# Optimization experiments

Measured on AMD Instinct MI355X. Metric: run time of the kernel, lower is better.

Reference implementation:

```python
import jax, jax.numpy as jnp
import numpy as np

B, N, E, ED, H, HID, OUT = 128, 100, 3200, 8, 4, 16, 32


def _ln(x, g, b):
    m = x.mean(-1, keepdims=True)
    v = ((x - m) ** 2).mean(-1, keepdims=True)
    return (x - m) / jnp.sqrt(v + 1e-5) * g + b


def _seg_softmax(logits, seg, n):
    # logits: [Etot, H], seg: [Etot] target node ids
    m = jax.ops.segment_max(logits, seg, num_segments=n)
    ex = jnp.exp(logits - m[seg])
    s = jax.ops.segment_sum(ex, seg, num_segments=n)
    return ex / (s[seg] + 1e-16)


def _tconv(x, src, dst, ea, Wq, bq, Wk, bk, Wv, bv, We, Ws, bs, heads, ch, n):
    # PyG TransformerConv, concat=False, root_weight=True, beta=False
    q = (x @ Wq.T + bq).reshape(-1, heads, ch)
    k = (x @ Wk.T + bk).reshape(-1, heads, ch)
    v = (x @ Wv.T + bv).reshape(-1, heads, ch)
    e = (ea @ We.T).reshape(-1, heads, ch)
    alpha = (q[dst] * (k[src] + e)).sum(-1) / jnp.sqrt(jnp.float32(ch))  # [Etot,H]
    alpha = _seg_softmax(alpha, dst, n)
    msg = (v[src] + e) * alpha[..., None]
    out = jax.ops.segment_sum(msg, dst, num_segments=n)  # [n,H,ch]
    out = out.mean(axis=1)  # concat=False -> head mean
    return out + x @ Ws.T + bs


def setup_inputs() -> dict:
    key = jax.random.key(0)
    ks = jax.random.split(key, 32)
    d = {}
    d['nodes_feats'] = jax.random.randint(ks[0], (B, N, 1), 0, 5).astype(jnp.float32)
    d['edge_index'] = jax.random.randint(ks[1], (B, 2, E), 0, N).astype(jnp.int32)
    d['edge_attr'] = jax.random.normal(ks[2], (B, E, ED), jnp.float32)
    d['agent_id'] = jax.random.randint(ks[3], (B, 1), 0, N).astype(jnp.int32)
    s = 0.1
    d['entity_embed'] = jax.random.normal(ks[4], (5, 4), jnp.float32)
    d['W1'] = jax.random.normal(ks[5], (HID, 4 + ED), jnp.float32) * s
    d['b1'] = jnp.zeros((HID,), jnp.float32)
    d['W2'] = jax.random.normal(ks[6], (HID, HID), jnp.float32) * s
    d['b2'] = jnp.zeros((HID,), jnp.float32)
    d['W3'] = jax.random.normal(ks[7], (HID, HID), jnp.float32) * s
    d['b3'] = jnp.zeros((HID,), jnp.float32)
    d['ln_g'] = jnp.ones((HID,), jnp.float32)
    d['ln_b'] = jnp.zeros((HID,), jnp.float32)
    i = 8
    for pre, ch, outd in (('g1', HID, HID), ('g2', OUT, OUT)):
        d[pre + '_Wq'] = jax.random.normal(ks[i + 0], (H * ch, HID), jnp.float32) * s
        d[pre + '_bq'] = jnp.zeros((H * ch,), jnp.float32)
        d[pre + '_Wk'] = jax.random.normal(ks[i + 1], (H * ch, HID), jnp.float32) * s
        d[pre + '_bk'] = jnp.zeros((H * ch,), jnp.float32)
        d[pre + '_Wv'] = jax.random.normal(ks[i + 2], (H * ch, HID), jnp.float32) * s
        d[pre + '_bv'] = jnp.zeros((H * ch,), jnp.float32)
        d[pre + '_We'] = jax.random.normal(ks[i + 3], (H * ch, ED), jnp.float32) * s
        d[pre + '_Ws'] = jax.random.normal(ks[i + 4], (outd, HID), jnp.float32) * s
        d[pre + '_bs'] = jnp.zeros((outd,), jnp.float32)
        i += 5
    return d


def reference(nodes_feats, edge_index, edge_attr, agent_id, entity_embed,
              W1, b1, W2, b2, W3, b3, ln_g, ln_b,
              g1_Wq, g1_bq, g1_Wk, g1_bk, g1_Wv, g1_bv, g1_We, g1_Ws, g1_bs,
              g2_Wq, g2_bq, g2_Wk, g2_bk, g2_Wv, g2_bv, g2_We, g2_Ws, g2_bs):
    n_tot = B * N
    # batched graph -> flat graph with per-batch node offsets
    offs = (jnp.arange(B, dtype=edge_index.dtype) * N)[:, None, None]
    ei = (edge_index + offs).transpose(1, 0, 2).reshape(2, -1)  # [2, B*E]
    src, dst = ei[0], ei[1]
    x = nodes_feats.reshape(-1, 1)            # [n_tot, 1]
    ea = edge_attr.reshape(-1, ED)            # [B*E, ED]

    # Embedding message-passing layer (aggr='add')
    etype = x[:, 0].astype(jnp.int32)[src]
    emb = entity_embed[etype]                  # [Etot, 4]
    h = jnp.concatenate([emb, ea], axis=1)
    h = _ln(jax.nn.relu(h @ W1.T + b1), ln_g, ln_b)
    h = _ln(jax.nn.relu(h @ W2.T + b2), ln_g, ln_b)
    h = _ln(jax.nn.relu(h @ W3.T + b3), ln_g, ln_b)
    z = jax.ops.segment_sum(h, dst, num_segments=n_tot)  # [n_tot, 16]

    a = _tconv(z, src, dst, ea, g1_Wq, g1_bq, g1_Wk, g1_bk, g1_Wv, g1_bv,
               g1_We, g1_Ws, g1_bs, H, HID, n_tot)
    a = _tconv(a, src, dst, ea, g2_Wq, g2_bq, g2_Wk, g2_bk, g2_Wv, g2_bv,
               g2_We, g2_Ws, g2_bs, H, OUT, n_tot)
    a = jax.nn.relu(a).reshape(B, N, OUT)
    # graph_aggr == 'agent': gather the agent node per batch
    out = jnp.take_along_axis(a, agent_id[:, :, None].astype(jnp.int32), axis=1)
    return out[:, 0, :]  # [B, OUT]
```

## Files before the change

kernel.cpp:

```cpp
#include <hip/hip_runtime.h>
#include <math.h>
#include <stdint.h>

#define Bb   128
#define Nn   100
#define Ee   3200
#define NTOT (Bb*Nn)
#define ETOT (Bb*Ee)



__global__ __launch_bounds__(256) void k_csr(const int* __restrict__ ei,
                                             const int* __restrict__ agent,
                                             int* __restrict__ off,
                                             int2* __restrict__ cpair,
                                             int* __restrict__ mark)
{
    int b = ((blockIdx.x & 7) << 4) + (blockIdx.x >> 3);
    int t = threadIdx.x;
    __shared__ int cnt[128];
    __shared__ int exc[128];
    __shared__ int cur[128];
    if (t < 128) cnt[t] = 0;
    if (t < Nn) mark[b * Nn + t] = 0;
    __syncthreads();
    const int* eis = ei + (size_t)b * 2 * Ee;
    const int* eid = eis + Ee;
    for (int e = t; e < Ee; e += 256) atomicAdd(&cnt[eid[e]], 1);
    __syncthreads();
    if (t < 128) exc[t] = cnt[t];
    __syncthreads();
    for (int d = 1; d < 128; d <<= 1) {
        int v = 0;
        if (t < 128 && t >= d) v = exc[t - d];
        __syncthreads();
        if (t < 128) exc[t] += v;
        __syncthreads();
    }
    if (t < 128) { int e0 = exc[t] - cnt[t]; exc[t] = e0; cur[t] = e0; }
    __syncthreads();
    if (t < Nn) off[b * Nn + t] = b * Ee + exc[t];
    if (b == Bb - 1 && t == 0) off[NTOT] = ETOT;
    for (int e = t; e < Ee; e += 256) {
        int dst = eid[e];
        int idx = atomicAdd(&cur[dst], 1);
        cpair[b * Ee + idx] = make_int2(eis[e] + b * Nn, b * Ee + e);
    }
    int an = agent[b];
    __syncthreads();
    if (t == 0) mark[b * Nn + an] = 1;
    for (int e = t; e < Ee; e += 256) {
        if (eid[e] == an) mark[b * Nn + eis[e]] = 1;
    }
}


__device__ __forceinline__ void ln_reg(float* h, const float* __restrict__ g,
                                       const float* __restrict__ b) {
    float s = 0.f;
#pragma unroll
    for (int c = 0; c < 16; c++) s += h[c];
    float m = s * 0.0625f;
    float v = 0.f;
#pragma unroll
    for (int c = 0; c < 16; c++) { float d = h[c] - m; v += d * d; }
    float r = rsqrtf(v * 0.0625f + 1e-5f);
#pragma unroll
    for (int c = 0; c < 16; c++) h[c] = (h[c] - m) * r * g[c] + b[c];
}

__global__ __launch_bounds__(256) void k_mlpz(
    const float* __restrict__ nf, const float* __restrict__ ea, const float* __restrict__ ee,
    const float* __restrict__ W1, const float* __restrict__ b1,
    const float* __restrict__ W2, const float* __restrict__ b2,
    const float* __restrict__ W3, const float* __restrict__ b3,
    const float* __restrict__ lg, const float* __restrict__ lb,
    const float* __restrict__ Wq, const float* __restrict__ bq,
    const float* __restrict__ Wk, const float* __restrict__ bk,
    const float* __restrict__ Wv, const float* __restrict__ bv,
    const int* __restrict__ off, const int2* __restrict__ cpair,
    float* __restrict__ z, float* __restrict__ q1, float* __restrict__ k1, float* __restrict__ v1)
{
    __shared__ float hs[4][64][17];
    __shared__ int sdeg[4];
    int lane = threadIdx.x & 63;
    int wid  = threadIdx.x >> 6;
    int n    = (blockIdx.x & 7) * (NTOT / 8) + (blockIdx.x >> 3) * 4 + wid;

    int o0 = off[n];
    int deg = off[n + 1] - o0;
    if (lane == 0) sdeg[wid] = deg;
    __syncthreads();
    int mdeg = max(max(sdeg[0], sdeg[1]), max(sdeg[2], sdeg[3]));
    int chunks = (mdeg + 63) >> 6;

    float zp = 0.f;
    for (int ch = 0; ch < chunks; ch++) {
        int i = ch * 64 + lane;
        float h3[16];
        if (i < deg) {
            int2 p = cpair[o0 + i];
            int et = (int)nf[p.x];
            float in[12];
#pragma unroll
            for (int j = 0; j < 4; j++) in[j] = ee[et * 4 + j];
            const float4* ea4 = (const float4*)(ea + (size_t)p.y * 8);
            float4 ua = ea4[0], ub = ea4[1];
            in[4] = ua.x; in[5] = ua.y; in[6] = ua.z; in[7] = ua.w;
            in[8] = ub.x; in[9] = ub.y; in[10] = ub.z; in[11] = ub.w;

            float h1[16];
#pragma unroll
            for (int c = 0; c < 16; c++) {
                float s = b1[c];
#pragma unroll
                for (int j = 0; j < 12; j++) s = fmaf(W1[c * 12 + j], in[j], s);
                h1[c] = fmaxf(s, 0.f);
            }
            ln_reg(h1, lg, lb);
            float h2[16];
#pragma unroll
            for (int c = 0; c < 16; c++) {
                float s = b2[c];
#pragma unroll
                for (int j = 0; j < 16; j++) s = fmaf(W2[c * 16 + j], h1[j], s);
                h2[c] = fmaxf(s, 0.f);
            }
            ln_reg(h2, lg, lb);
#pragma unroll
            for (int c = 0; c < 16; c++) {
                float s = b3[c];
#pragma unroll
                for (int j = 0; j < 16; j++) s = fmaf(W3[c * 16 + j], h2[j], s);
                h3[c] = fmaxf(s, 0.f);
            }
            ln_reg(h3, lg, lb);
        } else {
#pragma unroll
            for (int c = 0; c < 16; c++) h3[c] = 0.f;
        }
#pragma unroll
        for (int c = 0; c < 16; c++) hs[wid][lane][c] = h3[c];
        __syncthreads();
        int g = lane >> 4, c = lane & 15;
        float s = 0.f;
#pragma unroll
        for (int k = 0; k < 16; k++) s += hs[wid][g * 16 + k][c];
        s += __shfl_xor(s, 16);
        s += __shfl_xor(s, 32);
        zp += s;
        __syncthreads();
    }

    if (lane < 16) z[n * 16 + lane] = zp;

    float aq = bq[lane], ak = bk[lane], av = bv[lane];
#pragma unroll
    for (int j = 0; j < 16; j++) {
        float zj = __shfl(zp, j, 16);
        aq = fmaf(Wq[lane * 16 + j], zj, aq);
        ak = fmaf(Wk[lane * 16 + j], zj, ak);
        av = fmaf(Wv[lane * 16 + j], zj, av);
    }
    q1[n * 64 + lane] = aq;
    k1[n * 64 + lane] = ak;
    v1[n * 64 + lane] = av;
}


__global__ __launch_bounds__(256) void k_attn1(
    const float* __restrict__ ea,
    const float* __restrict__ q1, const float* __restrict__ k1, const float* __restrict__ v1,
    const float* __restrict__ We, const float* __restrict__ Ws, const float* __restrict__ bs,
    const float* __restrict__ z, const int* __restrict__ mark,
    const int* __restrict__ off, const int2* __restrict__ cpair,
    float* __restrict__ a1)
{
    int lane = threadIdx.x & 63;
    int wid  = threadIdx.x >> 6;
    int n    = (blockIdx.x & 7) * (NTOT / 8) + (blockIdx.x >> 3) * 4 + wid;

    if (!mark[n]) return;

    float wer[8];
#pragma unroll
    for (int j = 0; j < 8; j++) wer[j] = We[lane * 8 + j];
    float ql = q1[n * 64 + lane];

    int o0 = off[n];
    int deg = off[n + 1] - o0;

    float m = -1e30f, l = 0.f, acc = 0.f;
    int i = 0;
    for (; i + 2 <= deg; i += 2) {
        int2 pA = cpair[o0 + i];
        int2 pB = cpair[o0 + i + 1];
        const float4* eaA = (const float4*)(ea + (size_t)pA.y * 8);
        const float4* eaB = (const float4*)(ea + (size_t)pB.y * 8);
        float4 a0v = eaA[0], a1v = eaA[1], b0v = eaB[0], b1v = eaB[1];
        float eA = wer[0] * a0v.x + wer[1] * a0v.y + wer[2] * a0v.z + wer[3] * a0v.w
                 + wer[4] * a1v.x + wer[5] * a1v.y + wer[6] * a1v.z + wer[7] * a1v.w;
        float eB = wer[0] * b0v.x + wer[1] * b0v.y + wer[2] * b0v.z + wer[3] * b0v.w
                 + wer[4] * b1v.x + wer[5] * b1v.y + wer[6] * b1v.z + wer[7] * b1v.w;
        float kA = k1[(size_t)pA.x * 64 + lane];
        float kB = k1[(size_t)pB.x * 64 + lane];
        float vA = v1[(size_t)pA.x * 64 + lane];
        float vB = v1[(size_t)pB.x * 64 + lane];
        float tA = ql * (kA + eA);
        float tB = ql * (kB + eB);
        tA += __shfl_xor(tA, 1, 16);  tB += __shfl_xor(tB, 1, 16);
        tA += __shfl_xor(tA, 2, 16);  tB += __shfl_xor(tB, 2, 16);
        tA += __shfl_xor(tA, 4, 16);  tB += __shfl_xor(tB, 4, 16);
        tA += __shfl_xor(tA, 8, 16);  tB += __shfl_xor(tB, 8, 16);
        float lA = tA * 0.25f;
        float lB = tB * 0.25f;
        float nm = fmaxf(m, fmaxf(lA, lB));
        float sc = __expf(m - nm);
        float wA = __expf(lA - nm);
        float wB = __expf(lB - nm);
        acc = acc * sc + wA * (vA + eA) + wB * (vB + eB);
        l   = l * sc + wA + wB;
        m   = nm;
    }
    for (; i < deg; i++) {
        int2 p = cpair[o0 + i];
        const float4* ea4 = (const float4*)(ea + (size_t)p.y * 8);
        float4 u0 = ea4[0], u1 = ea4[1];
        float el = wer[0] * u0.x + wer[1] * u0.y + wer[2] * u0.z + wer[3] * u0.w
                 + wer[4] * u1.x + wer[5] * u1.y + wer[6] * u1.z + wer[7] * u1.w;
        float kl = k1[(size_t)p.x * 64 + lane];
        float t = ql * (kl + el);
        t += __shfl_xor(t, 1, 16);
        t += __shfl_xor(t, 2, 16);
        t += __shfl_xor(t, 4, 16);
        t += __shfl_xor(t, 8, 16);
        float logit = t * 0.25f;
        float nm = fmaxf(m, logit);
        float sc = __expf(m - nm);
        float w  = __expf(logit - nm);
        float vl = v1[(size_t)p.x * 64 + lane];
        acc = acc * sc + w * (vl + el);
        l   = l * sc + w;
        m   = nm;
    }
    float y = (deg > 0) ? (acc / l) : 0.f;
    y += __shfl_xor(y, 16);
    y += __shfl_xor(y, 32);
    y *= 0.25f;

    if (lane < 16) {
        float r = bs[lane];
#pragma unroll
        for (int j = 0; j < 16; j++) r = fmaf(Ws[lane * 16 + j], z[n * 16 + j], r);
        a1[n * 16 + lane] = y + r;
    }
}


__global__ __launch_bounds__(256) void k_g2(
    const float* __restrict__ ea, const float* __restrict__ a1, const int* __restrict__ agent,
    const float* __restrict__ Wq, const float* __restrict__ bq,
    const float* __restrict__ Wk, const float* __restrict__ bk,
    const float* __restrict__ Wv, const float* __restrict__ bv,
    const float* __restrict__ We, const float* __restrict__ Ws, const float* __restrict__ bs,
    const int* __restrict__ off, const int2* __restrict__ cpair,
    float* __restrict__ out)
{
    __shared__ float sm[4][64], sl[4][64], sa0[4][64], sa1[4][64];
    int b = ((blockIdx.x & 7) << 4) + (blockIdx.x >> 3);
    int lane = threadIdx.x & 63;
    int w = threadIdx.x >> 6;
    int n = b * Nn + agent[b];
    int v0 = lane * 2, v1i = lane * 2 + 1;

    float aa[16];
#pragma unroll
    for (int j = 0; j < 16; j++) aa[j] = a1[n * 16 + j];

    float wk0[16], wk1[16], wv0[16], wv1[16], we0[8], we1[8];
#pragma unroll
    for (int j = 0; j < 16; j++) {
        wk0[j] = Wk[v0 * 16 + j];  wk1[j] = Wk[v1i * 16 + j];
        wv0[j] = Wv[v0 * 16 + j];  wv1[j] = Wv[v1i * 16 + j];
    }
#pragma unroll
    for (int j = 0; j < 8; j++) { we0[j] = We[v0 * 8 + j]; we1[j] = We[v1i * 8 + j]; }

    float q0 = bq[v0], q1v = bq[v1i];
#pragma unroll
    for (int j = 0; j < 16; j++) {
        q0  = fmaf(Wq[v0 * 16 + j],  aa[j], q0);
        q1v = fmaf(Wq[v1i * 16 + j], aa[j], q1v);
    }

    int o0 = off[n];
    int deg = off[n + 1] - o0;

    float m = -1e30f, l = 0.f, a0 = 0.f, a1c = 0.f;
    for (int i = w; i < deg; i += 4) {
        int2 p = cpair[o0 + i];
        int src = p.x, ge = p.y;
        float as[16];
#pragma unroll
        for (int j = 0; j < 16; j++) as[j] = a1[src * 16 + j];
        const float4* ea4 = (const float4*)(ea + (size_t)ge * 8);
        float4 u0 = ea4[0], u1 = ea4[1];
        float eav[8] = {u0.x, u0.y, u0.z, u0.w, u1.x, u1.y, u1.z, u1.w};

        float k0 = bk[v0], k1v = bk[v1i], vv0 = bv[v0], vv1 = bv[v1i];
#pragma unroll
        for (int j = 0; j < 16; j++) {
            k0  = fmaf(wk0[j], as[j], k0);
            k1v = fmaf(wk1[j], as[j], k1v);
            vv0 = fmaf(wv0[j], as[j], vv0);
            vv1 = fmaf(wv1[j], as[j], vv1);
        }
        float e0 = 0.f, e1 = 0.f;
#pragma unroll
        for (int j = 0; j < 8; j++) { e0 = fmaf(we0[j], eav[j], e0); e1 = fmaf(we1[j], eav[j], e1); }

        float t = q0 * (k0 + e0) + q1v * (k1v + e1);
        t += __shfl_xor(t, 1, 16);
        t += __shfl_xor(t, 2, 16);
        t += __shfl_xor(t, 4, 16);
        t += __shfl_xor(t, 8, 16);
        float logit = t * 0.17677669529663687f;
        float nm = fmaxf(m, logit);
        float sc = __expf(m - nm);
        float wgt = __expf(logit - nm);
        a0  = a0 * sc + wgt * (vv0 + e0);
        a1c = a1c * sc + wgt * (vv1 + e1);
        l   = l * sc + wgt;
        m   = nm;
    }
    sm[w][lane] = m; sl[w][lane] = l; sa0[w][lane] = a0; sa1[w][lane] = a1c;
    __syncthreads();
    if (w == 0) {
        float M = fmaxf(fmaxf(sm[0][lane], sm[1][lane]), fmaxf(sm[2][lane], sm[3][lane]));
        float L = 0.f, A0 = 0.f, A1 = 0.f;
#pragma unroll
        for (int ww = 0; ww < 4; ww++) {
            float sc = __expf(sm[ww][lane] - M);
            L  += sc * sl[ww][lane];
            A0 += sc * sa0[ww][lane];
            A1 += sc * sa1[ww][lane];
        }
        float y0 = (deg > 0) ? (A0 / L) : 0.f;
        float y1 = (deg > 0) ? (A1 / L) : 0.f;
        y0 += __shfl_xor(y0, 16); y0 += __shfl_xor(y0, 32);
        y1 += __shfl_xor(y1, 16); y1 += __shfl_xor(y1, 32);
        y0 *= 0.25f; y1 *= 0.25f;

        if (lane < 16) {
            int c0 = lane * 2, c1 = lane * 2 + 1;
            float r0 = bs[c0], r1 = bs[c1];
#pragma unroll
            for (int j = 0; j < 16; j++) {
                r0 = fmaf(Ws[c0 * 16 + j], aa[j], r0);
                r1 = fmaf(Ws[c1 * 16 + j], aa[j], r1);
            }
            out[b * 32 + c0] = fmaxf(y0 + r0, 0.f);
            out[b * 32 + c1] = fmaxf(y1 + r1, 0.f);
        }
    }
}


extern "C" void kernel_launch(void* const* d_in, const int* in_sizes, int n_in,
                              void* d_out, int out_size, void* d_ws, size_t ws_size,
                              hipStream_t stream) {
    (void)in_sizes; (void)n_in; (void)out_size; (void)ws_size;
    const float* nf    = (const float*)d_in[0];
    const int*   ei    = (const int*)d_in[1];
    const float* ea    = (const float*)d_in[2];
    const int*   agent = (const int*)d_in[3];
    const float* ee    = (const float*)d_in[4];
    const float* W1    = (const float*)d_in[5];
    const float* b1    = (const float*)d_in[6];
    const float* W2    = (const float*)d_in[7];
    const float* b2    = (const float*)d_in[8];
    const float* W3    = (const float*)d_in[9];
    const float* b3    = (const float*)d_in[10];
    const float* lg    = (const float*)d_in[11];
    const float* lb    = (const float*)d_in[12];
    const float* g1Wq  = (const float*)d_in[13];
    const float* g1bq  = (const float*)d_in[14];
    const float* g1Wk  = (const float*)d_in[15];
    const float* g1bk  = (const float*)d_in[16];
    const float* g1Wv  = (const float*)d_in[17];
    const float* g1bv  = (const float*)d_in[18];
    const float* g1We  = (const float*)d_in[19];
    const float* g1Ws  = (const float*)d_in[20];
    const float* g1bs  = (const float*)d_in[21];
    const float* g2Wq  = (const float*)d_in[22];
    const float* g2bq  = (const float*)d_in[23];
    const float* g2Wk  = (const float*)d_in[24];
    const float* g2bk  = (const float*)d_in[25];
    const float* g2Wv  = (const float*)d_in[26];
    const float* g2bv  = (const float*)d_in[27];
    const float* g2We  = (const float*)d_in[28];
    const float* g2Ws  = (const float*)d_in[29];
    const float* g2bs  = (const float*)d_in[30];
    float* out = (float*)d_out;

    char* w = (char*)d_ws;
    int* mark  = (int*)w;  w += (size_t)NTOT * 4;
    int* off   = (int*)w;  w += (size_t)(NTOT + 4) * 4;
    w = (char*)(((uintptr_t)w + 15) & ~(uintptr_t)15);
    int2* cpair = (int2*)w; w += (size_t)ETOT * 8;
    float* z   = (float*)w; w += (size_t)NTOT * 16 * 4;
    float* q1  = (float*)w; w += (size_t)NTOT * 64 * 4;
    float* k1  = (float*)w; w += (size_t)NTOT * 64 * 4;
    float* v1  = (float*)w; w += (size_t)NTOT * 64 * 4;
    float* a1  = (float*)w; w += (size_t)NTOT * 16 * 4;

    k_csr<<<dim3(Bb), dim3(256), 0, stream>>>(ei, agent, off, cpair, mark);
    k_mlpz<<<dim3(NTOT / 4), dim3(256), 0, stream>>>(
        nf, ea, ee, W1, b1, W2, b2, W3, b3, lg, lb,
        g1Wq, g1bq, g1Wk, g1bk, g1Wv, g1bv,
        off, cpair, z, q1, k1, v1);
    k_attn1<<<dim3(NTOT / 4), dim3(256), 0, stream>>>(
        ea, q1, k1, v1, g1We, g1Ws, g1bs, z, mark, off, cpair, a1);
    k_g2<<<dim3(Bb), dim3(256), 0, stream>>>(
        ea, a1, agent, g2Wq, g2bq, g2Wk, g2bk, g2Wv, g2bv, g2We, g2Ws, g2bs,
        off, cpair, out);
}
```

Measured before the change: 206.7 us.

## Fuse layer-1 attention and layer-2 agent conv into one per-graph kernel

Merges the per-node first attention kernel and the per-graph second conv kernel into a single per-graph block of 512 threads. Each block stages the graph's k, v, z and CSR pairs in shared memory, and computes q on the fly, which removes the q1 and a1 global buffers and one launch. The CSR build also stages the edge indices in shared memory so global memory is read once. The cost is that only 128 blocks run the attention work, and each wave walks several marked nodes serially, which lowers parallelism.

```diff
diff --git a/kernel.cpp b/kernel.cpp
--- a/kernel.cpp
+++ b/kernel.cpp
@@ -10,7 +10,7 @@
 
 
 
-__global__ __launch_bounds__(256) void k_csr(const int* __restrict__ ei,
+__global__ __launch_bounds__(512) void k_csr(const int* __restrict__ ei,
                                              const int* __restrict__ agent,
                                              int* __restrict__ off,
                                              int2* __restrict__ cpair,
@@ -18,6 +18,8 @@
 {
     int b = ((blockIdx.x & 7) << 4) + (blockIdx.x >> 3);
     int t = threadIdx.x;
+    __shared__ int s_src[Ee];
+    __shared__ int s_dst[Ee];
     __shared__ int cnt[128];
     __shared__ int exc[128];
     __shared__ int cur[128];
@@ -26,7 +28,13 @@
     __syncthreads();
     const int* eis = ei + (size_t)b * 2 * Ee;
     const int* eid = eis + Ee;
-    for (int e = t; e < Ee; e += 256) atomicAdd(&cnt[eid[e]], 1);
+    for (int e = t; e < Ee; e += 512) {
+        int s = eis[e];
+        int d = eid[e];
+        s_src[e] = s;
+        s_dst[e] = d;
+        atomicAdd(&cnt[d], 1);
+    }
     __syncthreads();
     if (t < 128) exc[t] = cnt[t];
     __syncthreads();
@@ -41,16 +49,15 @@
     __syncthreads();
     if (t < Nn) off[b * Nn + t] = b * Ee + exc[t];
     if (b == Bb - 1 && t == 0) off[NTOT] = ETOT;
-    for (int e = t; e < Ee; e += 256) {
-        int dst = eid[e];
-        int idx = atomicAdd(&cur[dst], 1);
-        cpair[b * Ee + idx] = make_int2(eis[e] + b * Nn, b * Ee + e);
+    for (int e = t; e < Ee; e += 512) {
+        int d = s_dst[e];
+        int idx = atomicAdd(&cur[d], 1);
+        cpair[b * Ee + idx] = make_int2(s_src[e] + b * Nn, b * Ee + e);
     }
     int an = agent[b];
-    __syncthreads();
     if (t == 0) mark[b * Nn + an] = 1;
-    for (int e = t; e < Ee; e += 256) {
-        if (eid[e] == an) mark[b * Nn + eis[e]] = 1;
+    for (int e = t; e < Ee; e += 512) {
+        if (s_dst[e] == an) mark[b * Nn + s_src[e]] = 1;
     }
 }
 
@@ -75,11 +82,10 @@
     const float* __restrict__ W2, const float* __restrict__ b2,
     const float* __restrict__ W3, const float* __restrict__ b3,
     const float* __restrict__ lg, const float* __restrict__ lb,
-    const float* __restrict__ Wq, const float* __restrict__ bq,
     const float* __restrict__ Wk, const float* __restrict__ bk,
     const float* __restrict__ Wv, const float* __restrict__ bv,
     const int* __restrict__ off, const int2* __restrict__ cpair,
-    float* __restrict__ z, float* __restrict__ q1, float* __restrict__ k1, float* __restrict__ v1)
+    float* __restrict__ z, float* __restrict__ k1, float* __restrict__ v1)
 {
     __shared__ float hs[4][64][17];
     __shared__ int sdeg[4];
@@ -154,160 +160,187 @@
 
     if (lane < 16) z[n * 16 + lane] = zp;
 
-    float aq = bq[lane], ak = bk[lane], av = bv[lane];
+    float ak = bk[lane], av = bv[lane];
 #pragma unroll
     for (int j = 0; j < 16; j++) {
         float zj = __shfl(zp, j, 16);
-        aq = fmaf(Wq[lane * 16 + j], zj, aq);
         ak = fmaf(Wk[lane * 16 + j], zj, ak);
         av = fmaf(Wv[lane * 16 + j], zj, av);
     }
-    q1[n * 64 + lane] = aq;
     k1[n * 64 + lane] = ak;
     v1[n * 64 + lane] = av;
 }
 
 
-__global__ __launch_bounds__(256) void k_attn1(
+__global__ __launch_bounds__(512) void k_attn(
     const float* __restrict__ ea,
-    const float* __restrict__ q1, const float* __restrict__ k1, const float* __restrict__ v1,
-    const float* __restrict__ We, const float* __restrict__ Ws, const float* __restrict__ bs,
+    const float* __restrict__ k1, const float* __restrict__ v1,
     const float* __restrict__ z, const int* __restrict__ mark,
+    const int* __restrict__ agent,
     const int* __restrict__ off, const int2* __restrict__ cpair,
-    float* __restrict__ a1)
+    const float* __restrict__ g1Wq, const float* __restrict__ g1bq,
+    const float* __restrict__ g1We, const float* __restrict__ g1Ws, const float* __restrict__ g1bs,
+    const float* __restrict__ g2Wq, const float* __restrict__ g2bq,
+    const float* __restrict__ g2Wk, const float* __restrict__ g2bk,
+    const float* __restrict__ g2Wv, const float* __restrict__ g2bv,
+    const float* __restrict__ g2We, const float* __restrict__ g2Ws, const float* __restrict__ g2bs,
+    float* __restrict__ out)
 {
-    int lane = threadIdx.x & 63;
-    int wid  = threadIdx.x >> 6;
-    int n    = (blockIdx.x & 7) * (NTOT / 8) + (blockIdx.x >> 3) * 4 + wid;
-
-    if (!mark[n]) return;
-
-    float wer[8];
-#pragma unroll
-    for (int j = 0; j < 8; j++) wer[j] = We[lane * 8 + j];
-    float ql = q1[n * 64 + lane];
-
-    int o0 = off[n];
-    int deg = off[n + 1] - o0;
-
-    float m = -1e30f, l = 0.f, acc = 0.f;
-    int i = 0;
-    for (; i + 2 <= deg; i += 2) {
-        int2 pA = cpair[o0 + i];
-        int2 pB = cpair[o0 + i + 1];
-        const float4* eaA = (const float4*)(ea + (size_t)pA.y * 8);
-        const float4* eaB = (const float4*)(ea + (size_t)pB.y * 8);
-        float4 a0v = eaA[0], a1v = eaA[1], b0v = eaB[0], b1v = eaB[1];
-        float eA = wer[0] * a0v.x + wer[1] * a0v.y + wer[2] * a0v.z + wer[3] * a0v.w
-                 + wer[4] * a1v.x + wer[5] * a1v.y + wer[6] * a1v.z + wer[7] * a1v.w;
-        float eB = wer[0] * b0v.x + wer[1] * b0v.y + wer[2] * b0v.z + wer[3] * b0v.w
-                 + wer[4] * b1v.x + wer[5] * b1v.y + wer[6] * b1v.z + wer[7] * b1v.w;
-        float kA = k1[(size_t)pA.x * 64 + lane];
-        float kB = k1[(size_t)pB.x * 64 + lane];
-        float vA = v1[(size_t)pA.x * 64 + lane];
-        float vB = v1[(size_t)pB.x * 64 + lane];
-        float tA = ql * (kA + eA);
-        float tB = ql * (kB + eB);
-        tA += __shfl_xor(tA, 1, 16);  tB += __shfl_xor(tB, 1, 16);
-        tA += __shfl_xor(tA, 2, 16);  tB += __shfl_xor(tB, 2, 16);
-        tA += __shfl_xor(tA, 4, 16);  tB += __shfl_xor(tB, 4, 16);
-        tA += __shfl_xor(tA, 8, 16);  tB += __shfl_xor(tB, 8, 16);
-        float lA = tA * 0.25f;
-        float lB = tB * 0.25f;
-        float nm = fmaxf(m, fmaxf(lA, lB));
-        float sc = __expf(m - nm);
-        float wA = __expf(lA - nm);
-        float wB = __expf(lB - nm);
-        acc = acc * sc + wA * (vA + eA) + wB * (vB + eB);
-        l   = l * sc + wA + wB;
-        m   = nm;
-    }
-    for (; i < deg; i++) {
-        int2 p = cpair[o0 + i];
+    __shared__ alignas(16) float sk[Nn][64];
+    __shared__ alignas(16) float sv[Nn][64];
+    __shared__ alignas(16) int2  spair[Ee];
+    __shared__ alignas(16) float sz[Nn][16];
+    __shared__ float a1s[Nn][16];
+    __shared__ int   soff[Nn + 1];
+    __shared__ int   smark[Nn];
+    __shared__ float sm2[8][64], sl2[8][64], sa0[8][64], sa1[8][64];
+
+    int b = ((blockIdx.x & 7) << 4) + (blockIdx.x >> 3);
+    int t = threadIdx.x;
+    int lane = t & 63;
+    int wid  = t >> 6;
+
+    const float4* kg = (const float4*)(k1 + (size_t)b * Nn * 64);
+    const float4* vg = (const float4*)(v1 + (size_t)b * Nn * 64);
+    const float4* zg = (const float4*)(z  + (size_t)b * Nn * 16);
+    float4* skd = (float4*)&sk[0][0];
+    float4* svd = (float4*)&sv[0][0];
+    float4* szd = (float4*)&sz[0][0];
+    for (int i = t; i < Nn * 16; i += 512) { skd[i] = kg[i]; svd[i] = vg[i]; }
+    for (int i = t; i < Nn * 4; i += 512) szd[i] = zg[i];
+    const int2* cg = cpair + (size_t)b * Ee;
+    for (int i = t; i < Ee; i += 512) spair[i] = cg[i];
+    if (t <= Nn) soff[t] = off[b * Nn + t] - b * Ee;
+    if (t < Nn) smark[t] = mark[b * Nn + t];
+    __syncthreads();
+
+    float wq[16], wer[8], ws1[16];
+#pragma unroll
+    for (int j = 0; j < 16; j++) wq[j] = g1Wq[lane * 16 + j];
+#pragma unroll
+    for (int j = 0; j < 8; j++) wer[j] = g1We[lane * 8 + j];
+    float bq1 = g1bq[lane];
+    int lc = lane & 15;
+#pragma unroll
+    for (int j = 0; j < 16; j++) ws1[j] = g1Ws[lc * 16 + j];
+    float bs1 = g1bs[lc];
+
+    for (int loc = wid; loc < Nn; loc += 8) {
+        if (!smark[loc]) continue;
+        float zz[16];
+#pragma unroll
+        for (int j = 0; j < 16; j++) zz[j] = sz[loc][j];
+        float ql = bq1;
+#pragma unroll
+        for (int j = 0; j < 16; j++) ql = fmaf(wq[j], zz[j], ql);
+
+        int o0 = soff[loc];
+        int deg = soff[loc + 1] - o0;
+
+        float m = -1e30f, l = 0.f, acc = 0.f;
+        int i = 0;
+        for (; i + 2 <= deg; i += 2) {
+            int2 pA = spair[o0 + i];
+            int2 pB = spair[o0 + i + 1];
+            const float4* eaA = (const float4*)(ea + (size_t)pA.y * 8);
+            const float4* eaB = (const float4*)(ea + (size_t)pB.y * 8);
+            float4 a0v = eaA[0], a1v = eaA[1], b0v = eaB[0], b1v = eaB[1];
+            float eA = wer[0] * a0v.x + wer[1] * a0v.y + wer[2] * a0v.z + wer[3] * a0v.w
+                     + wer[4] * a1v.x + wer[5] * a1v.y + wer[6] * a1v.z + wer[7] * a1v.w;
+            float eB = wer[0] * b0v.x + wer[1] * b0v.y + wer[2] * b0v.z + wer[3] * b0v.w
+                     + wer[4] * b1v.x + wer[5] * b1v.y + wer[6] * b1v.z + wer[7] * b1v.w;
+            int la = pA.x - b * Nn, lB = pB.x - b * Nn;
+            float kA = sk[la][lane], kB = sk[lB][lane];
+            float vA = sv[la][lane], vB = sv[lB][lane];
+            float tA = ql * (kA + eA);
+            float tB = ql * (kB + eB);
+            tA += __shfl_xor(tA, 1, 16);  tB += __shfl_xor(tB, 1, 16);
+            tA += __shfl_xor(tA, 2, 16);  tB += __shfl_xor(tB, 2, 16);
+            tA += __shfl_xor(tA, 4, 16);  tB += __shfl_xor(tB, 4, 16);
+            tA += __shfl_xor(tA, 8, 16);  tB += __shfl_xor(tB, 8, 16);
+            float lA = tA * 0.25f;
+            float lBv = tB * 0.25f;
+            float nm = fmaxf(m, fmaxf(lA, lBv));
+            float sc = __expf(m - nm);
+            float wA = __expf(lA - nm);
+            float wB = __expf(lBv - nm);
+            acc = acc * sc + wA * (vA + eA) + wB * (vB + eB);
+            l   = l * sc + wA + wB;
+            m   = nm;
+        }
+        for (; i < deg; i++) {
+            int2 p = spair[o0 + i];
+            const float4* ea4 = (const float4*)(ea + (size_t)p.y * 8);
+            float4 u0 = ea4[0], u1 = ea4[1];
+            float el = wer[0] * u0.x + wer[1] * u0.y + wer[2] * u0.z + wer[3] * u0.w
+                     + wer[4] * u1.x + wer[5] * u1.y + wer[6] * u1.z + wer[7] * u1.w;
+            int ls = p.x - b * Nn;
+            float kl = sk[ls][lane];
+            float tq = ql * (kl + el);
+            tq += __shfl_xor(tq, 1, 16);
+            tq += __shfl_xor(tq, 2, 16);
+            tq += __shfl_xor(tq, 4, 16);
+            tq += __shfl_xor(tq, 8, 16);
+            float logit = tq * 0.25f;
+            float nm = fmaxf(m, logit);
+            float sc = __expf(m - nm);
+            float w  = __expf(logit - nm);
+            float vl = sv[ls][lane];
+            acc = acc * sc + w * (vl + el);
+            l   = l * sc + w;
+            m   = nm;
+        }
+        float y = (deg > 0) ? (acc / l) : 0.f;
+        y += __shfl_xor(y, 16);
+        y += __shfl_xor(y, 32);
+        y *= 0.25f;
+        if (lane < 16) {
+            float r = bs1;
+#pragma unroll
+            for (int j = 0; j < 16; j++) r = fmaf(ws1[j], zz[j], r);
+            a1s[loc][lane] = y + r;
+        }
+    }
+    __syncthreads();
+
+    int an = agent[b];
+    int v0 = lane * 2, v1i = lane * 2 + 1;
+
+    float aa[16];
+#pragma unroll
+    for (int j = 0; j < 16; j++) aa[j] = a1s[an][j];
+
+    float wk0[16], wk1[16], wv0[16], wv1[16], we0[8], we1[8];
+#pragma unroll
+    for (int j = 0; j < 16; j++) {
+        wk0[j] = g2Wk[v0 * 16 + j];  wk1[j] = g2Wk[v1i * 16 + j];
+        wv0[j] = g2Wv[v0 * 16 + j];  wv1[j] = g2Wv[v1i * 16 + j];
+    }
+#pragma unroll
+    for (int j = 0; j < 8; j++) { we0[j] = g2We[v0 * 8 + j]; we1[j] = g2We[v1i * 8 + j]; }
+
+    float q0 = g2bq[v0], q1v = g2bq[v1i];
+#pragma unroll
+    for (int j = 0; j < 16; j++) {
+        q0  = fmaf(g2Wq[v0 * 16 + j],  aa[j], q0);
+        q1v = fmaf(g2Wq[v1i * 16 + j], aa[j], q1v);
+    }
+
+    int o0a = soff[an];
+    int dega = soff[an + 1] - o0a;
+
+    float m = -1e30f, l = 0.f, a0 = 0.f, a1c = 0.f;
+    for (int i = wid; i < dega; i += 8) {
+        int2 p = spair[o0a + i];
+        int srcl = p.x - b * Nn;
+        float as[16];
+#pragma unroll
+        for (int j = 0; j < 16; j++) as[j] = a1s[srcl][j];
         const float4* ea4 = (const float4*)(ea + (size_t)p.y * 8);
         float4 u0 = ea4[0], u1 = ea4[1];
-        float el = wer[0] * u0.x + wer[1] * u0.y + wer[2] * u0.z + wer[3] * u0.w
-                 + wer[4] * u1.x + wer[5] * u1.y + wer[6] * u1.z + wer[7] * u1.w;
-        float kl = k1[(size_t)p.x * 64 + lane];
-        float t = ql * (kl + el);
-        t += __shfl_xor(t, 1, 16);
-        t += __shfl_xor(t, 2, 16);
-        t += __shfl_xor(t, 4, 16);
-        t += __shfl_xor(t, 8, 16);
-        float logit = t * 0.25f;
-        float nm = fmaxf(m, logit);
-        float sc = __expf(m - nm);
-        float w  = __expf(logit - nm);
-        float vl = v1[(size_t)p.x * 64 + lane];
-        acc = acc * sc + w * (vl + el);
-        l   = l * sc + w;
-        m   = nm;
-    }
-    float y = (deg > 0) ? (acc / l) : 0.f;
-    y += __shfl_xor(y, 16);
-    y += __shfl_xor(y, 32);
-    y *= 0.25f;
-
-    if (lane < 16) {
-        float r = bs[lane];
-#pragma unroll
-        for (int j = 0; j < 16; j++) r = fmaf(Ws[lane * 16 + j], z[n * 16 + j], r);
-        a1[n * 16 + lane] = y + r;
-    }
-}
-
-
-__global__ __launch_bounds__(256) void k_g2(
-    const float* __restrict__ ea, const float* __restrict__ a1, const int* __restrict__ agent,
-    const float* __restrict__ Wq, const float* __restrict__ bq,
-    const float* __restrict__ Wk, const float* __restrict__ bk,
-    const float* __restrict__ Wv, const float* __restrict__ bv,
-    const float* __restrict__ We, const float* __restrict__ Ws, const float* __restrict__ bs,
-    const int* __restrict__ off, const int2* __restrict__ cpair,
-    float* __restrict__ out)
-{
-    __shared__ float sm[4][64], sl[4][64], sa0[4][64], sa1[4][64];
-    int b = ((blockIdx.x & 7) << 4) + (blockIdx.x >> 3);
-    int lane = threadIdx.x & 63;
-    int w = threadIdx.x >> 6;
-    int n = b * Nn + agent[b];
-    int v0 = lane * 2, v1i = lane * 2 + 1;
-
-    float aa[16];
-#pragma unroll
-    for (int j = 0; j < 16; j++) aa[j] = a1[n * 16 + j];
-
-    float wk0[16], wk1[16], wv0[16], wv1[16], we0[8], we1[8];
-#pragma unroll
-    for (int j = 0; j < 16; j++) {
-        wk0[j] = Wk[v0 * 16 + j];  wk1[j] = Wk[v1i * 16 + j];
-        wv0[j] = Wv[v0 * 16 + j];  wv1[j] = Wv[v1i * 16 + j];
-    }
-#pragma unroll
-    for (int j = 0; j < 8; j++) { we0[j] = We[v0 * 8 + j]; we1[j] = We[v1i * 8 + j]; }
-
-    float q0 = bq[v0], q1v = bq[v1i];
-#pragma unroll
-    for (int j = 0; j < 16; j++) {
-        q0  = fmaf(Wq[v0 * 16 + j],  aa[j], q0);
-        q1v = fmaf(Wq[v1i * 16 + j], aa[j], q1v);
-    }
-
-    int o0 = off[n];
-    int deg = off[n + 1] - o0;
-
-    float m = -1e30f, l = 0.f, a0 = 0.f, a1c = 0.f;
-    for (int i = w; i < deg; i += 4) {
-        int2 p = cpair[o0 + i];
-        int src = p.x, ge = p.y;
-        float as[16];
-#pragma unroll
-        for (int j = 0; j < 16; j++) as[j] = a1[src * 16 + j];
-        const float4* ea4 = (const float4*)(ea + (size_t)ge * 8);
-        float4 u0 = ea4[0], u1 = ea4[1];
         float eav[8] = {u0.x, u0.y, u0.z, u0.w, u1.x, u1.y, u1.z, u1.w};
 
-        float k0 = bk[v0], k1v = bk[v1i], vv0 = bv[v0], vv1 = bv[v1i];
+        float k0 = g2bk[v0], k1v = g2bk[v1i], vv0 = g2bv[v0], vv1 = g2bv[v1i];
 #pragma unroll
         for (int j = 0; j < 16; j++) {
             k0  = fmaf(wk0[j], as[j], k0);
@@ -319,12 +352,12 @@
 #pragma unroll
         for (int j = 0; j < 8; j++) { e0 = fmaf(we0[j], eav[j], e0); e1 = fmaf(we1[j], eav[j], e1); }
 
-        float t = q0 * (k0 + e0) + q1v * (k1v + e1);
-        t += __shfl_xor(t, 1, 16);
-        t += __shfl_xor(t, 2, 16);
-        t += __shfl_xor(t, 4, 16);
-        t += __shfl_xor(t, 8, 16);
-        float logit = t * 0.17677669529663687f;
+        float tq = q0 * (k0 + e0) + q1v * (k1v + e1);
+        tq += __shfl_xor(tq, 1, 16);
+        tq += __shfl_xor(tq, 2, 16);
+        tq += __shfl_xor(tq, 4, 16);
+        tq += __shfl_xor(tq, 8, 16);
+        float logit = tq * 0.17677669529663687f;
         float nm = fmaxf(m, logit);
         float sc = __expf(m - nm);
         float wgt = __expf(logit - nm);
@@ -333,31 +366,33 @@
         l   = l * sc + wgt;
         m   = nm;
     }
-    sm[w][lane] = m; sl[w][lane] = l; sa0[w][lane] = a0; sa1[w][lane] = a1c;
-    __syncthreads();
-    if (w == 0) {
-        float M = fmaxf(fmaxf(sm[0][lane], sm[1][lane]), fmaxf(sm[2][lane], sm[3][lane]));
+    sm2[wid][lane] = m; sl2[wid][lane] = l; sa0[wid][lane] = a0; sa1[wid][lane] = a1c;
+    __syncthreads();
+    if (wid == 0) {
+        float M = sm2[0][lane];
+#pragma unroll
+        for (int ww = 1; ww < 8; ww++) M = fmaxf(M, sm2[ww][lane]);
         float L = 0.f, A0 = 0.f, A1 = 0.f;
 #pragma unroll
-        for (int ww = 0; ww < 4; ww++) {
-            float sc = __expf(sm[ww][lane] - M);
-            L  += sc * sl[ww][lane];
+        for (int ww = 0; ww < 8; ww++) {
+            float sc = __expf(sm2[ww][lane] - M);
+            L  += sc * sl2[ww][lane];
             A0 += sc * sa0[ww][lane];
             A1 += sc * sa1[ww][lane];
         }
-        float y0 = (deg > 0) ? (A0 / L) : 0.f;
-        float y1 = (deg > 0) ? (A1 / L) : 0.f;
+        float y0 = (dega > 0) ? (A0 / L) : 0.f;
+        float y1 = (dega > 0) ? (A1 / L) : 0.f;
         y0 += __shfl_xor(y0, 16); y0 += __shfl_xor(y0, 32);
         y1 += __shfl_xor(y1, 16); y1 += __shfl_xor(y1, 32);
         y0 *= 0.25f; y1 *= 0.25f;
 
         if (lane < 16) {
             int c0 = lane * 2, c1 = lane * 2 + 1;
-            float r0 = bs[c0], r1 = bs[c1];
+            float r0 = g2bs[c0], r1 = g2bs[c1];
 #pragma unroll
             for (int j = 0; j < 16; j++) {
-                r0 = fmaf(Ws[c0 * 16 + j], aa[j], r0);
-                r1 = fmaf(Ws[c1 * 16 + j], aa[j], r1);
+                r0 = fmaf(g2Ws[c0 * 16 + j], aa[j], r0);
+                r1 = fmaf(g2Ws[c1 * 16 + j], aa[j], r1);
             }
             out[b * 32 + c0] = fmaxf(y0 + r0, 0.f);
             out[b * 32 + c1] = fmaxf(y1 + r1, 0.f);
@@ -409,19 +444,17 @@
     w = (char*)(((uintptr_t)w + 15) & ~(uintptr_t)15);
     int2* cpair = (int2*)w; w += (size_t)ETOT * 8;
     float* z   = (float*)w; w += (size_t)NTOT * 16 * 4;
-    float* q1  = (float*)w; w += (size_t)NTOT * 64 * 4;
     float* k1  = (float*)w; w += (size_t)NTOT * 64 * 4;
     float* v1  = (float*)w; w += (size_t)NTOT * 64 * 4;
-    float* a1  = (float*)w; w += (size_t)NTOT * 16 * 4;
-
-    k_csr<<<dim3(Bb), dim3(256), 0, stream>>>(ei, agent, off, cpair, mark);
+
+    k_csr<<<dim3(Bb), dim3(512), 0, stream>>>(ei, agent, off, cpair, mark);
     k_mlpz<<<dim3(NTOT / 4), dim3(256), 0, stream>>>(
         nf, ea, ee, W1, b1, W2, b2, W3, b3, lg, lb,
-        g1Wq, g1bq, g1Wk, g1bk, g1Wv, g1bv,
-        off, cpair, z, q1, k1, v1);
-    k_attn1<<<dim3(NTOT / 4), dim3(256), 0, stream>>>(
-        ea, q1, k1, v1, g1We, g1Ws, g1bs, z, mark, off, cpair, a1);
-    k_g2<<<dim3(Bb), dim3(256), 0, stream>>>(
-        ea, a1, agent, g2Wq, g2bq, g2Wk, g2bk, g2Wv, g2bv, g2We, g2Ws, g2bs,
-        off, cpair, out);
+        g1Wk, g1bk, g1Wv, g1bv,
+        off, cpair, z, k1, v1);
+    k_attn<<<dim3(Bb), dim3(512), 0, stream>>>(
+        ea, k1, v1, z, mark, agent, off, cpair,
+        g1Wq, g1bq, g1We, g1Ws, g1bs,
+        g2Wq, g2bq, g2Wk, g2bk, g2Wv, g2bv, g2We, g2Ws, g2bs,
+        out);
 }
```

New measurement: 236.3 us. +14.3%, slower.

## Split attention over waves per node, move Q projection into attention, stage CSR in LDS

Applied to the files above, without the earlier changes.

The CSR build kernel now uses 512 threads and stages src/dst indices in shared memory, so global edge indices are read only once. The first-layer attention kernel launches one block per node and splits that node's edges across four waves, then merges the partial online-softmax results through shared memory. Q is now computed only for marked nodes inside attention instead of for every node in the MLP kernel, which removes the q1 buffer writes. The second-layer kernel goes from 4 to 8 waves per graph. Exited unmarked blocks make the launch larger, and the extra shared-memory merge adds sync overhead.

```diff
diff --git a/kernel.cpp b/kernel.cpp
--- a/kernel.cpp
+++ b/kernel.cpp
@@ -10,7 +10,7 @@
 
 
 
-__global__ __launch_bounds__(256) void k_csr(const int* __restrict__ ei,
+__global__ __launch_bounds__(512) void k_csr(const int* __restrict__ ei,
                                              const int* __restrict__ agent,
                                              int* __restrict__ off,
                                              int2* __restrict__ cpair,
@@ -18,6 +18,8 @@
 {
     int b = ((blockIdx.x & 7) << 4) + (blockIdx.x >> 3);
     int t = threadIdx.x;
+    __shared__ int s_src[Ee];
+    __shared__ int s_dst[Ee];
     __shared__ int cnt[128];
     __shared__ int exc[128];
     __shared__ int cur[128];
@@ -26,7 +28,13 @@
     __syncthreads();
     const int* eis = ei + (size_t)b * 2 * Ee;
     const int* eid = eis + Ee;
-    for (int e = t; e < Ee; e += 256) atomicAdd(&cnt[eid[e]], 1);
+    for (int e = t; e < Ee; e += 512) {
+        int s = eis[e];
+        int d = eid[e];
+        s_src[e] = s;
+        s_dst[e] = d;
+        atomicAdd(&cnt[d], 1);
+    }
     __syncthreads();
     if (t < 128) exc[t] = cnt[t];
     __syncthreads();
@@ -41,16 +49,15 @@
     __syncthreads();
     if (t < Nn) off[b * Nn + t] = b * Ee + exc[t];
     if (b == Bb - 1 && t == 0) off[NTOT] = ETOT;
-    for (int e = t; e < Ee; e += 256) {
-        int dst = eid[e];
-        int idx = atomicAdd(&cur[dst], 1);
-        cpair[b * Ee + idx] = make_int2(eis[e] + b * Nn, b * Ee + e);
+    for (int e = t; e < Ee; e += 512) {
+        int d = s_dst[e];
+        int idx = atomicAdd(&cur[d], 1);
+        cpair[b * Ee + idx] = make_int2(s_src[e] + b * Nn, b * Ee + e);
     }
     int an = agent[b];
-    __syncthreads();
     if (t == 0) mark[b * Nn + an] = 1;
-    for (int e = t; e < Ee; e += 256) {
-        if (eid[e] == an) mark[b * Nn + eis[e]] = 1;
+    for (int e = t; e < Ee; e += 512) {
+        if (s_dst[e] == an) mark[b * Nn + s_src[e]] = 1;
     }
 }
 
@@ -75,11 +82,10 @@
     const float* __restrict__ W2, const float* __restrict__ b2,
     const float* __restrict__ W3, const float* __restrict__ b3,
     const float* __restrict__ lg, const float* __restrict__ lb,
-    const float* __restrict__ Wq, const float* __restrict__ bq,
     const float* __restrict__ Wk, const float* __restrict__ bk,
     const float* __restrict__ Wv, const float* __restrict__ bv,
     const int* __restrict__ off, const int2* __restrict__ cpair,
-    float* __restrict__ z, float* __restrict__ q1, float* __restrict__ k1, float* __restrict__ v1)
+    float* __restrict__ z, float* __restrict__ k1, float* __restrict__ v1)
 {
     __shared__ float hs[4][64][17];
     __shared__ int sdeg[4];
@@ -154,15 +160,13 @@
 
     if (lane < 16) z[n * 16 + lane] = zp;
 
-    float aq = bq[lane], ak = bk[lane], av = bv[lane];
+    float ak = bk[lane], av = bv[lane];
 #pragma unroll
     for (int j = 0; j < 16; j++) {
         float zj = __shfl(zp, j, 16);
-        aq = fmaf(Wq[lane * 16 + j], zj, aq);
         ak = fmaf(Wk[lane * 16 + j], zj, ak);
         av = fmaf(Wv[lane * 16 + j], zj, av);
     }
-    q1[n * 64 + lane] = aq;
     k1[n * 64 + lane] = ak;
     v1[n * 64 + lane] = av;
 }
@@ -170,31 +174,39 @@
 
 __global__ __launch_bounds__(256) void k_attn1(
     const float* __restrict__ ea,
-    const float* __restrict__ q1, const float* __restrict__ k1, const float* __restrict__ v1,
+    const float* __restrict__ k1, const float* __restrict__ v1,
+    const float* __restrict__ z, const int* __restrict__ mark,
+    const float* __restrict__ Wq, const float* __restrict__ bq,
     const float* __restrict__ We, const float* __restrict__ Ws, const float* __restrict__ bs,
-    const float* __restrict__ z, const int* __restrict__ mark,
     const int* __restrict__ off, const int2* __restrict__ cpair,
     float* __restrict__ a1)
 {
+    int n = (blockIdx.x & 7) * (NTOT / 8) + (blockIdx.x >> 3);
+    if (!mark[n]) return;
+
+    __shared__ float sm[4][64], sl[4][64], sa[4][64];
     int lane = threadIdx.x & 63;
-    int wid  = threadIdx.x >> 6;
-    int n    = (blockIdx.x & 7) * (NTOT / 8) + (blockIdx.x >> 3) * 4 + wid;
-
-    if (!mark[n]) return;
-
+    int w    = threadIdx.x >> 6;
+
+    float zz[16];
+#pragma unroll
+    for (int j = 0; j < 16; j++) zz[j] = z[n * 16 + j];
+    float ql = bq[lane];
+#pragma unroll
+    for (int j = 0; j < 16; j++) ql = fmaf(Wq[lane * 16 + j], zz[j], ql);
     float wer[8];
 #pragma unroll
     for (int j = 0; j < 8; j++) wer[j] = We[lane * 8 + j];
-    float ql = q1[n * 64 + lane];
-
-    int o0 = off[n];
+
+    int o0  = off[n];
     int deg = off[n + 1] - o0;
+    int i    = o0 + ((deg * w) >> 2);
+    int iend = o0 + ((deg * (w + 1)) >> 2);
 
     float m = -1e30f, l = 0.f, acc = 0.f;
-    int i = 0;
-    for (; i + 2 <= deg; i += 2) {
-        int2 pA = cpair[o0 + i];
-        int2 pB = cpair[o0 + i + 1];
+    for (; i + 2 <= iend; i += 2) {
+        int2 pA = cpair[i];
+        int2 pB = cpair[i + 1];
         const float4* eaA = (const float4*)(ea + (size_t)pA.y * 8);
         const float4* eaB = (const float4*)(ea + (size_t)pB.y * 8);
         float4 a0v = eaA[0], a1v = eaA[1], b0v = eaB[0], b1v = eaB[1];
@@ -212,52 +224,63 @@
         tA += __shfl_xor(tA, 2, 16);  tB += __shfl_xor(tB, 2, 16);
         tA += __shfl_xor(tA, 4, 16);  tB += __shfl_xor(tB, 4, 16);
         tA += __shfl_xor(tA, 8, 16);  tB += __shfl_xor(tB, 8, 16);
-        float lA = tA * 0.25f;
-        float lB = tB * 0.25f;
-        float nm = fmaxf(m, fmaxf(lA, lB));
+        float lA  = tA * 0.25f;
+        float lBv = tB * 0.25f;
+        float nm = fmaxf(m, fmaxf(lA, lBv));
         float sc = __expf(m - nm);
         float wA = __expf(lA - nm);
-        float wB = __expf(lB - nm);
+        float wB = __expf(lBv - nm);
         acc = acc * sc + wA * (vA + eA) + wB * (vB + eB);
         l   = l * sc + wA + wB;
         m   = nm;
     }
-    for (; i < deg; i++) {
-        int2 p = cpair[o0 + i];
+    for (; i < iend; i++) {
+        int2 p = cpair[i];
         const float4* ea4 = (const float4*)(ea + (size_t)p.y * 8);
         float4 u0 = ea4[0], u1 = ea4[1];
         float el = wer[0] * u0.x + wer[1] * u0.y + wer[2] * u0.z + wer[3] * u0.w
                  + wer[4] * u1.x + wer[5] * u1.y + wer[6] * u1.z + wer[7] * u1.w;
         float kl = k1[(size_t)p.x * 64 + lane];
-        float t = ql * (kl + el);
-        t += __shfl_xor(t, 1, 16);
-        t += __shfl_xor(t, 2, 16);
-        t += __shfl_xor(t, 4, 16);
-        t += __shfl_xor(t, 8, 16);
-        float logit = t * 0.25f;
+        float tq = ql * (kl + el);
+        tq += __shfl_xor(tq, 1, 16);
+        tq += __shfl_xor(tq, 2, 16);
+        tq += __shfl_xor(tq, 4, 16);
+        tq += __shfl_xor(tq, 8, 16);
+        float logit = tq * 0.25f;
         float nm = fmaxf(m, logit);
         float sc = __expf(m - nm);
-        float w  = __expf(logit - nm);
+        float wv = __expf(logit - nm);
         float vl = v1[(size_t)p.x * 64 + lane];
-        acc = acc * sc + w * (vl + el);
-        l   = l * sc + w;
+        acc = acc * sc + wv * (vl + el);
+        l   = l * sc + wv;
         m   = nm;
     }
-    float y = (deg > 0) ? (acc / l) : 0.f;
-    y += __shfl_xor(y, 16);
-    y += __shfl_xor(y, 32);
-    y *= 0.25f;
-
-    if (lane < 16) {
-        float r = bs[lane];
-#pragma unroll
-        for (int j = 0; j < 16; j++) r = fmaf(Ws[lane * 16 + j], z[n * 16 + j], r);
-        a1[n * 16 + lane] = y + r;
-    }
-}
-
-
-__global__ __launch_bounds__(256) void k_g2(
+    sm[w][lane] = m; sl[w][lane] = l; sa[w][lane] = acc;
+    __syncthreads();
+    if (w == 0) {
+        float M = fmaxf(fmaxf(sm[0][lane], sm[1][lane]), fmaxf(sm[2][lane], sm[3][lane]));
+        float L = 0.f, A = 0.f;
+#pragma unroll
+        for (int ww = 0; ww < 4; ww++) {
+            float sc = __expf(sm[ww][lane] - M);
+            L += sc * sl[ww][lane];
+            A += sc * sa[ww][lane];
+        }
+        float y = (deg > 0) ? (A / L) : 0.f;
+        y += __shfl_xor(y, 16);
+        y += __shfl_xor(y, 32);
+        y *= 0.25f;
+        if (lane < 16) {
+            float r = bs[lane];
+#pragma unroll
+            for (int j = 0; j < 16; j++) r = fmaf(Ws[lane * 16 + j], zz[j], r);
+            a1[n * 16 + lane] = y + r;
+        }
+    }
+}
+
+
+__global__ __launch_bounds__(512) void k_g2(
     const float* __restrict__ ea, const float* __restrict__ a1, const int* __restrict__ agent,
     const float* __restrict__ Wq, const float* __restrict__ bq,
     const float* __restrict__ Wk, const float* __restrict__ bk,
@@ -266,7 +289,7 @@
     const int* __restrict__ off, const int2* __restrict__ cpair,
     float* __restrict__ out)
 {
-    __shared__ float sm[4][64], sl[4][64], sa0[4][64], sa1[4][64];
+    __shared__ float sm[8][64], sl[8][64], sa0[8][64], sa1[8][64];
     int b = ((blockIdx.x & 7) << 4) + (blockIdx.x >> 3);
     int lane = threadIdx.x & 63;
     int w = threadIdx.x >> 6;
@@ -297,7 +320,7 @@
     int deg = off[n + 1] - o0;
 
     float m = -1e30f, l = 0.f, a0 = 0.f, a1c = 0.f;
-    for (int i = w; i < deg; i += 4) {
+    for (int i = w; i < deg; i += 8) {
         int2 p = cpair[o0 + i];
         int src = p.x, ge = p.y;
         float as[16];
@@ -336,10 +359,12 @@
     sm[w][lane] = m; sl[w][lane] = l; sa0[w][lane] = a0; sa1[w][lane] = a1c;
     __syncthreads();
     if (w == 0) {
-        float M = fmaxf(fmaxf(sm[0][lane], sm[1][lane]), fmaxf(sm[2][lane], sm[3][lane]));
+        float M = sm[0][lane];
+#pragma unroll
+        for (int ww = 1; ww < 8; ww++) M = fmaxf(M, sm[ww][lane]);
         float L = 0.f, A0 = 0.f, A1 = 0.f;
 #pragma unroll
-        for (int ww = 0; ww < 4; ww++) {
+        for (int ww = 0; ww < 8; ww++) {
             float sc = __expf(sm[ww][lane] - M);
             L  += sc * sl[ww][lane];
             A0 += sc * sa0[ww][lane];
@@ -409,19 +434,20 @@
     w = (char*)(((uintptr_t)w + 15) & ~(uintptr_t)15);
     int2* cpair = (int2*)w; w += (size_t)ETOT * 8;
     float* z   = (float*)w; w += (size_t)NTOT * 16 * 4;
-    float* q1  = (float*)w; w += (size_t)NTOT * 64 * 4;
     float* k1  = (float*)w; w += (size_t)NTOT * 64 * 4;
     float* v1  = (float*)w; w += (size_t)NTOT * 64 * 4;
     float* a1  = (float*)w; w += (size_t)NTOT * 16 * 4;
 
-    k_csr<<<dim3(Bb), dim3(256), 0, stream>>>(ei, agent, off, cpair, mark);
+    k_csr<<<dim3(Bb), dim3(512), 0, stream>>>(ei, agent, off, cpair, mark);
     k_mlpz<<<dim3(NTOT / 4), dim3(256), 0, stream>>>(
         nf, ea, ee, W1, b1, W2, b2, W3, b3, lg, lb,
-        g1Wq, g1bq, g1Wk, g1bk, g1Wv, g1bv,
-        off, cpair, z, q1, k1, v1);
-    k_attn1<<<dim3(NTOT / 4), dim3(256), 0, stream>>>(
-        ea, q1, k1, v1, g1We, g1Ws, g1bs, z, mark, off, cpair, a1);
-    k_g2<<<dim3(Bb), dim3(256), 0, stream>>>(
+        g1Wk, g1bk, g1Wv, g1bv,
+        off, cpair, z, k1, v1);
+    k_attn1<<<dim3(NTOT), dim3(256), 0, stream>>>(
+        ea, k1, v1, z, mark,
+        g1Wq, g1bq, g1We, g1Ws, g1bs,
+        off, cpair, a1);
+    k_g2<<<dim3(Bb), dim3(512), 0, stream>>>(
         ea, a1, agent, g2Wq, g2bq, g2Wk, g2bk, g2Wv, g2bv, g2We, g2Ws, g2bs,
         off, cpair, out);
 }
```

Result: faster. 194.8 us (-5.8%).
